# Kernel tuning notes

Measured on AMD Instinct MI355X. Metric: run time of the kernel, lower is better.

Reference implementation:

```python
import jax, jax.numpy as jnp
import numpy as np

B, F = 65536, 300
SIGMA = 2.0
ALPHA = 1.0


def _gaussian_kernel(sigma):
    l = int(np.round(3 * sigma + 1.0))  # 7 for sigma=2
    x = np.linspace(-(l - 1.0) / 2.0, (l - 1.0) / 2.0, l)
    k = np.exp(-0.5 * np.square(x) / np.square(sigma))
    return (k / k.sum()).astype(np.float32)


def setup_inputs() -> dict:
    key = jax.random.key(0)
    fr_funcs = jax.random.normal(key, (B, F), dtype=jnp.float32)
    freqs = np.arange(1, F + 1, dtype=np.float32)
    freqs = (freqs - freqs.min()) / (freqs.max() - freqs.min())
    freqs = freqs * 2.0 - 1.0  # normalized to [-1, 1], as in __init__
    return {
        "fr_funcs": fr_funcs,
        "freqs": jnp.asarray(freqs),
        "kernel": jnp.asarray(_gaussian_kernel(SIGMA)),
    }


def _first_peak_loss(f, freqs):
    # Replicates softlocalmax's first segment.
    # find_peaks on symmetric-padded signal => boundary is a peak iff it
    # strictly exceeds its single neighbor; interior peaks are strict local maxima.
    n = f.shape[0]
    interior = (f[1:-1] > f[:-2]) & (f[1:-1] > f[2:])
    is_peak = jnp.concatenate([f[0:1] > f[1:2], interior, f[-1:] > f[-2:-1]])
    idx = jnp.where(is_peak, jnp.arange(n, dtype=jnp.int32), n)
    two = jnp.sort(idx)[:2]  # first two peak positions (n if absent)
    npeaks = jnp.sum(is_peak.astype(jnp.int32))
    # first segment end: midpoint of first two peaks (int truncation), else n-1
    end = jnp.where(npeaks >= 2, (two[0] + two[1]) // 2, n - 1)
    mask = jnp.arange(n) < end
    logits = jnp.where(mask, f * ALPHA, -jnp.inf)
    w = jax.nn.softmax(logits)  # zeros outside segment == softmax over slice
    softargmax = w @ freqs
    return -softargmax


def reference(fr_funcs, freqs, kernel):
    # Gaussian1DBlur: conv1d with padding='same' (zero padding, odd kernel)
    blurred = jax.lax.conv_general_dilated(
        fr_funcs[:, None, :], kernel[None, None, :], (1,), "SAME"
    )[:, 0]  # (B, F)
    return jax.vmap(_first_peak_loss, in_axes=(0, None))(blurred, freqs)
```

## Files before the change

### kernel.cpp

```cpp
#include <hip/hip_runtime.h>
#include <math.h>

#define NF 300
#define NC 75
#define CH 14
#define BL (4*CH-4)

#define CONV(b0,b1,b2,b3,c0,c1,c2,A,B) \
    b0 = kk[0]*c0;  b0=fmaf(kk[1],c1 ,b0); b0=fmaf(kk[2],c2 ,b0); b0=fmaf(kk[3],A.x,b0); b0=fmaf(kk[4],A.y,b0); b0=fmaf(kk[5],A.z,b0); b0=fmaf(kk[6],A.w,b0); \
    b1 = kk[0]*c1;  b1=fmaf(kk[1],c2 ,b1); b1=fmaf(kk[2],A.x,b1); b1=fmaf(kk[3],A.y,b1); b1=fmaf(kk[4],A.z,b1); b1=fmaf(kk[5],A.w,b1); b1=fmaf(kk[6],B.x,b1); \
    b2 = kk[0]*c2;  b2=fmaf(kk[1],A.x,b2); b2=fmaf(kk[2],A.y,b2); b2=fmaf(kk[3],A.z,b2); b2=fmaf(kk[4],A.w,b2); b2=fmaf(kk[5],B.x,b2); b2=fmaf(kk[6],B.y,b2); \
    b3 = kk[0]*A.x; b3=fmaf(kk[1],A.y,b3); b3=fmaf(kk[2],A.z,b3); b3=fmaf(kk[3],A.w,b3); b3=fmaf(kk[4],B.x,b3); b3=fmaf(kk[5],B.y,b3); b3=fmaf(kk[6],B.z,b3);

#define PKCHK(J) { if (cnt==0) p0=(J); else if (cnt==1) p1=(J); ++cnt; }

__global__ __launch_bounds__(256, 1) void peak_mover_loss_kernel(
    const float* __restrict__ in,
    const float* __restrict__ freqs,
    const float* __restrict__ kw,
    float* __restrict__ out)
{
    const int row = blockIdx.x * blockDim.x + threadIdx.x;
    const float4* rp4 = reinterpret_cast<const float4*>(in + (size_t)row * NF);
    (void)freqs;

    float4 ch[CH];
#pragma unroll
    for (int t = 0; t < CH; ++t) ch[t] = rp4[t];

    float kk[7];
#pragma unroll
    for (int t = 0; t < 7; ++t) kk[t] = kw[t];

    float bl[BL];
    float c0 = 0.f, c1 = 0.f, c2 = 0.f;
    float prev1 = -INFINITY, prev2 = -INFINITY;
    int cnt = 0, p0 = 0, p1 = 0;
#pragma unroll
    for (int m = 0; m < CH - 1; ++m) {
        if (m >= 2 && (m & 1) == 0) { if (__all(cnt >= 2)) break; }
        float b0, b1, b2, b3;
        CONV(b0, b1, b2, b3, c0, c1, c2, ch[m], ch[m + 1]);
        bl[4*m] = b0; bl[4*m+1] = b1; bl[4*m+2] = b2; bl[4*m+3] = b3;
        const int base = 4 * m;
        if (prev1 > prev2 && prev1 > b0) PKCHK(base - 1)
        if (b0 > prev1 && b0 > b1)       PKCHK(base)
        if (b1 > b0 && b1 > b2)          PKCHK(base + 1)
        if (b2 > b1 && b2 > b3)          PKCHK(base + 2)
        prev2 = b2; prev1 = b3;
        c0 = ch[m].y; c1 = ch[m].z; c2 = ch[m].w;
    }
    float4 A4 = ch[CH - 1];

    int mc = CH - 1;
#pragma unroll 1
    while (cnt < 2 && mc < NC) {
        float4 cc[17];
        cc[0] = A4;
#pragma unroll
        for (int t = 1; t <= 16; ++t) {
            const int idx = mc + t;
            float4 v = make_float4(0.f, 0.f, 0.f, 0.f);
            if (idx < NC) v = rp4[idx];
            cc[t] = v;
        }
#pragma unroll
        for (int t = 0; t < 16; ++t) {
            const int m = mc + t;
            if (m < NC && cnt < 2) {
                float b0, b1, b2, b3;
                CONV(b0, b1, b2, b3, c0, c1, c2, cc[t], cc[t + 1]);
                const int base = 4 * m;
                if (prev1 > prev2 && prev1 > b0) PKCHK(base - 1)
                if (b0 > prev1 && b0 > b1)       PKCHK(base)
                if (b1 > b0 && b1 > b2)          PKCHK(base + 1)
                if (b2 > b1 && b2 > b3)          PKCHK(base + 2)
                if (m == NC - 1 && cnt < 2 && b3 > b2) PKCHK(NF - 1)
                prev2 = b2; prev1 = b3;
                c0 = cc[t].y; c1 = cc[t].z; c2 = cc[t].w;
            }
        }
        A4 = cc[16];
        mc += 16;
    }

    const int end = (cnt >= 2) ? ((p0 + p1) >> 1) : (NF - 1);

    const float fsc = 2.0f / 299.0f;
    float s = 0.f, tt = 0.f;
    if (end <= BL) {
#pragma unroll
        for (int jb = 0; jb < BL; jb += 4) {
            if (!__any(jb < end)) break;
#pragma unroll
            for (int e = 0; e < 4; ++e) {
                const int j = jb + e;
                if (j < end) {
                    const float ev = __expf(bl[j]);
                    s += ev;
                    tt = fmaf(ev, fmaf((float)j, fsc, -1.f), tt);
                }
            }
        }
    } else {
        float d0 = 0.f, d1 = 0.f, d2 = 0.f;
        float4 A = rp4[0], B = rp4[1], C = rp4[2], D = rp4[3];
        int m = 0;
#pragma unroll 1
        while (4 * m < end) {
            float b0, b1, b2, b3;
            CONV(b0, b1, b2, b3, d0, d1, d2, A, B);
            const int base = 4 * m;
            if (base     < end) { float e=__expf(b0); s+=e; tt=fmaf(e, fmaf((float)(base  ), fsc, -1.f), tt); }
            if (base + 1 < end) { float e=__expf(b1); s+=e; tt=fmaf(e, fmaf((float)(base+1), fsc, -1.f), tt); }
            if (base + 2 < end) { float e=__expf(b2); s+=e; tt=fmaf(e, fmaf((float)(base+2), fsc, -1.f), tt); }
            if (base + 3 < end) { float e=__expf(b3); s+=e; tt=fmaf(e, fmaf((float)(base+3), fsc, -1.f), tt); }
            d0 = A.y; d1 = A.z; d2 = A.w;
            A = B; B = C; C = D;
            const int k = m + 4;
            float4 nd = make_float4(0.f, 0.f, 0.f, 0.f);
            if (k < NC) nd = rp4[k];
            D = nd;
            ++m;
        }
    }

    out[row] = -(tt / s);
}

extern "C" void kernel_launch(void* const* d_in, const int* in_sizes, int n_in,
                              void* d_out, int out_size, void* d_ws, size_t ws_size,
                              hipStream_t stream) {
    const float* fr    = (const float*)d_in[0];
    const float* freqs = (const float*)d_in[1];
    const float* kw    = (const float*)d_in[2];
    float* outp = (float*)d_out;

    const int nrows = in_sizes[0] / NF;
    const int block = 256;
    const int grid  = nrows / block;
    peak_mover_loss_kernel<<<grid, block, 0, stream>>>(fr, freqs, kw, outp);
}
```

Measured before the change: 105.4 us.

## Split each row across four lanes with shuffle-merged peak search

Instead of one thread per row, four adjacent lanes now share a row. Each lane blurs and peak-scans its own 16-sample slice (the last lane takes 20), then the lanes merge their first-two-peak results with xor shuffles. The softmax partial sums are reduced across the four lanes the same way. Launch bounds rise to 4 blocks per CU and the grid grows fourfold, aiming for more parallelism, better-coalesced loads and lower register pressure. The cost is shuffle overhead, a larger thread count, and redundant work in the rare far-peak fallback, where every lane computes the full row.

```diff
diff --git a/kernel.cpp b/kernel.cpp
--- a/kernel.cpp
+++ b/kernel.cpp
@@ -3,8 +3,7 @@
 
 #define NF 300
 #define NC 75
-#define CH 14
-#define BL (4*CH-4)
+#define G 4
 
 #define CONV(b0,b1,b2,b3,c0,c1,c2,A,B) \
     b0 = kk[0]*c0;  b0=fmaf(kk[1],c1 ,b0); b0=fmaf(kk[2],c2 ,b0); b0=fmaf(kk[3],A.x,b0); b0=fmaf(kk[4],A.y,b0); b0=fmaf(kk[5],A.z,b0); b0=fmaf(kk[6],A.w,b0); \
@@ -14,91 +13,126 @@
 
 #define PKCHK(J) { if (cnt==0) p0=(J); else if (cnt==1) p1=(J); ++cnt; }
 
-__global__ __launch_bounds__(256, 1) void peak_mover_loss_kernel(
+__global__ __launch_bounds__(256, 4) void peak_mover_loss_kernel(
     const float* __restrict__ in,
     const float* __restrict__ freqs,
     const float* __restrict__ kw,
     float* __restrict__ out)
 {
-    const int row = blockIdx.x * blockDim.x + threadIdx.x;
+    const int tid = threadIdx.x;
+    const int l   = tid & (G - 1);
+    const int row = blockIdx.x * (256 / G) + (tid >> 2);
     const float4* rp4 = reinterpret_cast<const float4*>(in + (size_t)row * NF);
     (void)freqs;
 
-    float4 ch[CH];
+    const int cbase = 4 * l - 2;
+    float4 ch[8];
 #pragma unroll
-    for (int t = 0; t < CH; ++t) ch[t] = rp4[t];
+    for (int t = 0; t < 8; ++t) {
+        const int idx = cbase + t;
+        float4 v = make_float4(0.f, 0.f, 0.f, 0.f);
+        if (idx >= 0) v = rp4[idx];
+        ch[t] = v;
+    }
 
     float kk[7];
 #pragma unroll
     for (int t = 0; t < 7; ++t) kk[t] = kw[t];
 
-    float bl[BL];
-    float c0 = 0.f, c1 = 0.f, c2 = 0.f;
-    float prev1 = -INFINITY, prev2 = -INFINITY;
+    float c0, c1, c2, prev1, prev2;
+    {
+        float pb0, pb1, pb2, pb3;
+        float h0 = ch[0].y, h1 = ch[0].z, h2 = ch[0].w;
+        CONV(pb0, pb1, pb2, pb3, h0, h1, h2, ch[1], ch[2]);
+        (void)pb0; (void)pb1;
+        prev2 = pb2; prev1 = pb3;
+        c0 = ch[1].y; c1 = ch[1].z; c2 = ch[1].w;
+        if (l == 0) { prev1 = -INFINITY; prev2 = -INFINITY; }
+    }
+
+    float bl[20];
     int cnt = 0, p0 = 0, p1 = 0;
 #pragma unroll
-    for (int m = 0; m < CH - 1; ++m) {
-        if (m >= 2 && (m & 1) == 0) { if (__all(cnt >= 2)) break; }
-        float b0, b1, b2, b3;
-        CONV(b0, b1, b2, b3, c0, c1, c2, ch[m], ch[m + 1]);
-        bl[4*m] = b0; bl[4*m+1] = b1; bl[4*m+2] = b2; bl[4*m+3] = b3;
-        const int base = 4 * m;
-        if (prev1 > prev2 && prev1 > b0) PKCHK(base - 1)
-        if (b0 > prev1 && b0 > b1)       PKCHK(base)
-        if (b1 > b0 && b1 > b2)          PKCHK(base + 1)
-        if (b2 > b1 && b2 > b3)          PKCHK(base + 2)
-        prev2 = b2; prev1 = b3;
-        c0 = ch[m].y; c1 = ch[m].z; c2 = ch[m].w;
+    for (int t = 0; t < 5; ++t) {
+        if (t < 4 || l == G - 1) {
+            float b0, b1, b2, b3;
+            CONV(b0, b1, b2, b3, c0, c1, c2, ch[2 + t], ch[3 + t]);
+            bl[4*t] = b0; bl[4*t+1] = b1; bl[4*t+2] = b2; bl[4*t+3] = b3;
+            const int base = 16 * l + 4 * t;
+            if (prev1 > prev2 && prev1 > b0) PKCHK(base - 1)
+            if (b0 > prev1 && b0 > b1)       PKCHK(base)
+            if (b1 > b0 && b1 > b2)          PKCHK(base + 1)
+            if (b2 > b1 && b2 > b3)          PKCHK(base + 2)
+            prev2 = b2; prev1 = b3;
+            c0 = ch[2+t].y; c1 = ch[2+t].z; c2 = ch[2+t].w;
+        }
     }
-    float4 A4 = ch[CH - 1];
 
-    int mc = CH - 1;
+#pragma unroll
+    for (int o = 1; o < G; o <<= 1) {
+        const int oc = __shfl_xor(cnt, o, G);
+        const int q0 = __shfl_xor(p0, o, G);
+        const int q1 = __shfl_xor(p1, o, G);
+        const bool right = (l & o) != 0;
+        const int Lc = right ? oc : cnt, Rc = right ? cnt : oc;
+        const int L0 = right ? q0 : p0,  R0 = right ? p0 : q0;
+        const int L1 = right ? q1 : p1,  R1 = right ? p1 : q1;
+        p0 = (Lc >= 1) ? L0 : R0;
+        p1 = (Lc >= 2) ? L1 : ((Lc == 1) ? R0 : R1);
+        cnt = (Lc + Rc < 2) ? (Lc + Rc) : 2;
+    }
+
+    if (cnt < 2) {
+        prev1 = __shfl(prev1, 3, G);
+        prev2 = __shfl(prev2, 3, G);
+        c0 = __shfl(c0, 3, G); c1 = __shfl(c1, 3, G); c2 = __shfl(c2, 3, G);
+        float4 A4 = rp4[17];
+        int mc = 17;
 #pragma unroll 1
-    while (cnt < 2 && mc < NC) {
-        float4 cc[17];
-        cc[0] = A4;
+        while (cnt < 2 && mc < NC) {
+            float4 cc[9];
+            cc[0] = A4;
 #pragma unroll
-        for (int t = 1; t <= 16; ++t) {
-            const int idx = mc + t;
-            float4 v = make_float4(0.f, 0.f, 0.f, 0.f);
-            if (idx < NC) v = rp4[idx];
-            cc[t] = v;
+            for (int t = 1; t <= 8; ++t) {
+                const int idx = mc + t;
+                float4 v = make_float4(0.f, 0.f, 0.f, 0.f);
+                if (idx < NC) v = rp4[idx];
+                cc[t] = v;
+            }
+#pragma unroll
+            for (int t = 0; t < 8; ++t) {
+                const int m = mc + t;
+                if (m < NC && cnt < 2) {
+                    float b0, b1, b2, b3;
+                    CONV(b0, b1, b2, b3, c0, c1, c2, cc[t], cc[t + 1]);
+                    const int base = 4 * m;
+                    if (prev1 > prev2 && prev1 > b0) PKCHK(base - 1)
+                    if (b0 > prev1 && b0 > b1)       PKCHK(base)
+                    if (b1 > b0 && b1 > b2)          PKCHK(base + 1)
+                    if (b2 > b1 && b2 > b3)          PKCHK(base + 2)
+                    if (m == NC - 1 && cnt < 2 && b3 > b2) PKCHK(NF - 1)
+                    prev2 = b2; prev1 = b3;
+                    c0 = cc[t].y; c1 = cc[t].z; c2 = cc[t].w;
+                }
+            }
+            A4 = cc[8];
+            mc += 8;
         }
-#pragma unroll
-        for (int t = 0; t < 16; ++t) {
-            const int m = mc + t;
-            if (m < NC && cnt < 2) {
-                float b0, b1, b2, b3;
-                CONV(b0, b1, b2, b3, c0, c1, c2, cc[t], cc[t + 1]);
-                const int base = 4 * m;
-                if (prev1 > prev2 && prev1 > b0) PKCHK(base - 1)
-                if (b0 > prev1 && b0 > b1)       PKCHK(base)
-                if (b1 > b0 && b1 > b2)          PKCHK(base + 1)
-                if (b2 > b1 && b2 > b3)          PKCHK(base + 2)
-                if (m == NC - 1 && cnt < 2 && b3 > b2) PKCHK(NF - 1)
-                prev2 = b2; prev1 = b3;
-                c0 = cc[t].y; c1 = cc[t].z; c2 = cc[t].w;
-            }
-        }
-        A4 = cc[16];
-        mc += 16;
     }
 
     const int end = (cnt >= 2) ? ((p0 + p1) >> 1) : (NF - 1);
 
     const float fsc = 2.0f / 299.0f;
     float s = 0.f, tt = 0.f;
-    if (end <= BL) {
+    if (end <= 68) {
 #pragma unroll
-        for (int jb = 0; jb < BL; jb += 4) {
-            if (!__any(jb < end)) break;
-#pragma unroll
-            for (int e = 0; e < 4; ++e) {
-                const int j = jb + e;
+        for (int t = 0; t < 20; ++t) {
+            if (t < 16 || l == G - 1) {
+                const int j = 16 * l + t;
                 if (j < end) {
-                    const float ev = __expf(bl[j]);
-                    s += ev;
-                    tt = fmaf(ev, fmaf((float)j, fsc, -1.f), tt);
+                    const float e = __expf(bl[t]);
+                    s += e;
+                    tt = fmaf(e, fmaf((float)j, fsc, -1.f), tt);
                 }
             }
         }
@@ -125,7 +159,12 @@
         }
     }
 
-    out[row] = -(tt / s);
+#pragma unroll
+    for (int o = 1; o < G; o <<= 1) {
+        s  += __shfl_xor(s,  o, G);
+        tt += __shfl_xor(tt, o, G);
+    }
+    if (l == 0) out[row] = -(tt / s);
 }
 
 extern "C" void kernel_launch(void* const* d_in, const int* in_sizes, int n_in,
@@ -138,6 +177,6 @@
 
     const int nrows = in_sizes[0] / NF;
     const int block = 256;
-    const int grid  = nrows / block;
+    const int grid  = (nrows * G) / block;
     peak_mover_loss_kernel<<<grid, block, 0, stream>>>(fr, freqs, kw, outp);
 }
```

New measurement: 108.5 us. +2.9%, slower.
